# Kernel tuning notes

Measured on AMD Instinct MI355X. Metric: run time of the kernel, lower is better.

The kernel has to match this reference:

```python
import jax, jax.numpy as jnp
import numpy as np

S, B, E = 4096, 8, 1024
H, D, K = 16, 64, 64  # num_heads, head_dim, proj_dim
TAU = 1.0

def setup_inputs() -> dict:
    key = jax.random.key(0)
    ks = jax.random.split(key, 6)
    return {
        "encoder_output": jax.random.normal(ks[0], (S, B, E), dtype=jnp.float32),
        "Wk": jax.random.normal(ks[1], (E, E), dtype=jnp.float32) * (E ** -0.5),
        "bk": jax.random.normal(ks[2], (E,), dtype=jnp.float32) * 0.02,
        "Wv": jax.random.normal(ks[3], (E, E), dtype=jnp.float32) * (E ** -0.5),
        "bv": jax.random.normal(ks[4], (E,), dtype=jnp.float32) * 0.02,
        "random_matrices": jax.random.normal(ks[5], (H, K, D), dtype=jnp.float32),
        "mask": jnp.zeros((S, B, 1, 1), dtype=bool),
    }

def reference(encoder_output, Wk, bk, Wv, bv, random_matrices, mask):
    # k/v projections: [S,B,E] -> [S,B,H,D]
    k = (encoder_output @ Wk.T + bk).reshape(S, B, H, D)
    v = (encoder_output @ Wv.T + bv).reshape(S, B, H, D)
    # build_random_matrices (reparam_proj=False): divide by tau
    rm = random_matrices / TAU
    # rrf random feature map: scale by head_dim**-0.5 / tau, project, sin/cos concat
    x = k * (D ** -0.5) / TAU
    proj = jnp.einsum('sbhd,hkd->sbhk', x, rm)  # [S,B,H,K]
    phi_k = jnp.concatenate([jnp.sin(proj), jnp.cos(proj)], axis=-1) * (K ** -0.5)  # [S,B,H,2K]
    phi_k = jnp.where(mask, 0.0, phi_k)
    # s/z linear-attention state accumulation over seq_len
    s = jnp.einsum('sbhk,sbhd->bhkd', phi_k, v)  # [B,H,2K,D]
    z = jnp.sum(phi_k, axis=0)                   # [B,H,2K]
    return (s, z, rm)
```

## Files before the change

kernel.cpp:

```cpp
#include <hip/hip_runtime.h>
#include <hip/hip_bf16.h>
#include <stdint.h>


typedef short bf16x8 __attribute__((ext_vector_type(8)));
typedef float f32x4 __attribute__((ext_vector_type(4)));

__device__ __forceinline__ unsigned short f2bf(float f) {
  unsigned u = __float_as_uint(f);
  u += 0x7fffu + ((u >> 16) & 1u);
  return (unsigned short)(u >> 16);
}
__device__ __forceinline__ unsigned pack2(float a, float b) {
  return (unsigned)f2bf(a) | ((unsigned)f2bf(b) << 16);
}

#define OFF_WC   0ull
#define OFF_BC   4194304ull
#define OFF_AB   4202496ull
#define OFF_PS   71311360ull
#define OFF_PZ   104865792ull

#define NB_CONV 16384
#define NB_W2   (NB_CONV + 256)
#define NB_WV   (NB_W2 + 512)
#define NB_RM   (NB_WV + 64)
#define NB_ALL  (NB_RM + 1)

__global__ __launch_bounds__(256) void k_pre(const float* __restrict__ enc,
                                             const float* __restrict__ Wk,
                                             const float* __restrict__ bk,
                                             const float* __restrict__ Wv,
                                             const float* __restrict__ bv,
                                             const float* __restrict__ rm,
                                             unsigned short* __restrict__ ab,
                                             unsigned short* __restrict__ Wc,
                                             float* __restrict__ bc,
                                             float* __restrict__ out) {
  const int bid = blockIdx.x;
  const int tid = threadIdx.x;
  if (bid < NB_CONV) {
    const int r = bid * 2 + (tid >> 7);
    const int e = (tid & 127) * 8;
    const int s = r >> 3, b = r & 7;
    const float4* p = (const float4*)(enc + (size_t)r * 1024 + e);
    float4 a = p[0], b4 = p[1];
    uint4 o;
    o.x = pack2(a.x, a.y);  o.y = pack2(a.z, a.w);
    o.z = pack2(b4.x, b4.y); o.w = pack2(b4.z, b4.w);
    *(uint4*)(ab + ((size_t)b * 4096 + s) * 1024 + e) = o;
  } else if (bid < NB_W2) {
    const int t = bid - NB_CONV;
    const int h = t >> 4, et = t & 15;
    __shared__ float Rt[64][65];
    __shared__ float Wt[64][65];
    #pragma unroll
    for (int i = 0; i < 4; ++i) {
      const int fi = i * 256 + tid;
      const int row = fi >> 4, c4 = (fi & 15) * 4;
      float4 w = *(const float4*)(Wk + (size_t)(h * 64 + row) * 1024 + et * 64 + c4);
      Wt[row][c4] = w.x; Wt[row][c4 + 1] = w.y; Wt[row][c4 + 2] = w.z; Wt[row][c4 + 3] = w.w;
      float4 r = *(const float4*)(rm + (size_t)(h * 64 + row) * 64 + c4);
      Rt[row][c4] = r.x * 0.125f; Rt[row][c4 + 1] = r.y * 0.125f;
      Rt[row][c4 + 2] = r.z * 0.125f; Rt[row][c4 + 3] = r.w * 0.125f;
    }
    __syncthreads();
    const int kk = tid & 63, eq = tid >> 6, e0 = eq * 16;
    float accw[16] = {};
    for (int d = 0; d < 64; ++d) {
      const float rv = Rt[kk][d];
      #pragma unroll
      for (int i = 0; i < 16; ++i) accw[i] += rv * Wt[d][e0 + i];
    }
    unsigned short* wout = Wc + (size_t)(h * 64 + kk) * 1024 + et * 64 + e0;
    #pragma unroll
    for (int i2 = 0; i2 < 4; ++i2) {
      uint2 o; o.x = pack2(accw[i2 * 4], accw[i2 * 4 + 1]);
      o.y = pack2(accw[i2 * 4 + 2], accw[i2 * 4 + 3]);
      *(uint2*)(wout + i2 * 4) = o;
    }
    if (et == 0 && tid < 64) {
      float sbb = 0.f;
      for (int d = 0; d < 64; ++d) sbb += Rt[tid][d] * bk[h * 64 + d];
      bc[h * 64 + tid] = sbb;
    }
  } else if (bid < NB_WV) {
    size_t i = ((size_t)(bid - NB_W2) * 256 + tid) * 8;
    const float4* p = (const float4*)(Wv + i);
    float4 a = p[0], b4 = p[1];
    uint4 o;
    o.x = pack2(a.x, a.y);  o.y = pack2(a.z, a.w);
    o.z = pack2(b4.x, b4.y); o.w = pack2(b4.z, b4.w);
    *(uint4*)(Wc + 1048576ull + i) = o;
  } else if (bid < NB_RM) {
    size_t i = ((size_t)(bid - NB_WV) * 256 + tid) * 4;
    *(float4*)(out + 1064960 + i) = *(const float4*)(rm + i);
  } else {
    const int j = tid * 4;
    if (j < 1024) *(float4*)(bc + 1024 + j) = *(const float4*)(bv + j);
  }
}

__device__ __forceinline__ void glds16(const unsigned short* g, unsigned short* l) {
  __builtin_amdgcn_global_load_lds((const __attribute__((address_space(1))) unsigned int*)g,
                                   (__attribute__((address_space(3))) unsigned int*)l,
                                   16, 0, 0);
}

__global__ __launch_bounds__(256, 2) void k_fused(const unsigned short* __restrict__ Ab,
                                                  const unsigned short* __restrict__ Wc,
                                                  const float* __restrict__ bc,
                                                  float* __restrict__ ps,
                                                  float* __restrict__ pz) {
  __shared__ char smem[50176];
  unsigned short* As = (unsigned short*)smem;
  unsigned short* Bs = As + 128 * 64;
  unsigned short* Ph = (unsigned short*)smem;
  unsigned short* Vl = (unsigned short*)(smem + 32768);
  float* zbuf = (float*)(smem + 49152);
  float* Psf  = (float*)smem;

  const int bx = blockIdx.x;
  const int xcd = bx & 7;
  const int idx = bx >> 3;
  const int hp = idx & 7;
  const int g = idx >> 3;
  const int bcg = g * 8 + xcd;
  const int b = bcg >> 3;
  const int sp = bcg & 7;

  const int tid = threadIdx.x;
  const int wave = tid >> 6;
  const int lane = tid & 63;
  const int wm = wave >> 1, wn = wave & 1;
  const int quad = lane >> 4, lm = lane & 15;
  const int lr = lane >> 3;
  const int lc = (((lane & 7) ^ lr) * 8);

  int nrow[4];
  #pragma unroll
  for (int j = 0; j < 4; ++j)
    nrow[j] = (j < 2) ? (wn * 32 + j * 16 + lm) : (64 + wn * 32 + (j - 2) * 16 + lm);
  float biasjh[2][4];
  #pragma unroll
  for (int hi = 0; hi < 2; ++hi) {
    const int h = hp * 2 + hi;
    #pragma unroll
    for (int j = 0; j < 4; ++j)
      biasjh[hi][j] = (j < 2) ? bc[h * 64 + nrow[j]] : bc[1024 + h * 64 + (nrow[j] - 64)];
  }

  f32x4 acc2[2][2][4] = {};
  float zsv[2][2] = {}, zcv[2][2] = {};

  for (int st = 0; st < 4; ++st) {
    const int s_base = sp * 512 + st * 128;
    for (int hi = 0; hi < 2; ++hi) {
      const int h = hp * 2 + hi;
      f32x4 acc[4][4] = {};

      for (int kt = 0; kt < 16; ++kt) {
        const int k0 = kt * 64;
        __syncthreads();
        #pragma unroll
        for (int c = 0; c < 4; ++c) {
          const int r = wave * 32 + c * 8;
          glds16(Ab + ((size_t)b * 4096 + s_base + r + lr) * 1024 + k0 + lc, &As[r * 64]);
          const int rr = r + lr;
          const int wrow = h * 64 + rr + ((rr >= 64) ? 960 : 0);
          glds16(Wc + (size_t)wrow * 1024 + k0 + lc, &Bs[r * 64]);
        }
        __syncthreads();
        #pragma unroll
        for (int ks = 0; ks < 2; ++ks) {
          bf16x8 af[4], bfr[4];
          const int sw = ((ks * 4 + quad) ^ (lm & 7)) * 8;
          #pragma unroll
          for (int i = 0; i < 4; ++i)
            af[i] = *(const bf16x8*)&As[(wm * 64 + i * 16 + lm) * 64 + sw];
          #pragma unroll
          for (int j = 0; j < 4; ++j)
            bfr[j] = *(const bf16x8*)&Bs[nrow[j] * 64 + sw];
          #pragma unroll
          for (int i = 0; i < 4; ++i)
            #pragma unroll
            for (int j = 0; j < 4; ++j)
              acc[i][j] = __builtin_amdgcn_mfma_f32_16x16x32_bf16(af[i], bfr[j], acc[i][j], 0, 0, 0);
        }
      }

      __syncthreads();
      #pragma unroll
      for (int j = 0; j < 4; ++j) {
        #pragma unroll
        for (int i = 0; i < 4; ++i) {
          const int ch = wm * 8 + i * 2 + (quad >> 1);
          const int half = (quad & 1) * 4;
          if (j < 2) {
            const int kk = wn * 32 + j * 16 + lm;
            float sv[4], cv[4];
            #pragma unroll
            for (int r = 0; r < 4; ++r) {
              float p = acc[i][j][r] + biasjh[hi][j];
              __sincosf(p, &sv[r], &cv[r]);
              sv[r] *= 0.125f; cv[r] *= 0.125f;
            }
            zsv[hi][j] += sv[0] + sv[1] + sv[2] + sv[3];
            zcv[hi][j] += cv[0] + cv[1] + cv[2] + cv[3];
            uint2 os; os.x = pack2(sv[0], sv[1]); os.y = pack2(sv[2], sv[3]);
            uint2 oc; oc.x = pack2(cv[0], cv[1]); oc.y = pack2(cv[2], cv[3]);
            const int chs = (ch ^ (kk & 7)) * 8;
            *(uint2*)&Ph[kk * 128 + chs + half] = os;
            *(uint2*)&Ph[(kk + 64) * 128 + chs + half] = oc;
          } else {
            const int d = wn * 32 + (j - 2) * 16 + lm;
            uint2 ov;
            ov.x = pack2(acc[i][j][0] + biasjh[hi][j], acc[i][j][1] + biasjh[hi][j]);
            ov.y = pack2(acc[i][j][2] + biasjh[hi][j], acc[i][j][3] + biasjh[hi][j]);
            *(uint2*)&Vl[d * 128 + ((ch ^ (d & 7)) * 8) + half] = ov;
          }
        }
      }
      __syncthreads();

      #pragma unroll
      for (int ks2 = 0; ks2 < 4; ++ks2) {
        bf16x8 pa[2], vb[4];
        #pragma unroll
        for (int i2 = 0; i2 < 2; ++i2) {
          const int c = wave * 32 + i2 * 16 + lm;
          pa[i2] = *(const bf16x8*)&Ph[c * 128 + (((ks2 * 4 + quad) ^ (c & 7)) * 8)];
        }
        #pragma unroll
        for (int j2 = 0; j2 < 4; ++j2) {
          const int d = j2 * 16 + lm;
          vb[j2] = *(const bf16x8*)&Vl[d * 128 + (((ks2 * 4 + quad) ^ (d & 7)) * 8)];
        }
        #pragma unroll
        for (int i2 = 0; i2 < 2; ++i2)
          #pragma unroll
          for (int j2 = 0; j2 < 4; ++j2)
            acc2[hi][i2][j2] = __builtin_amdgcn_mfma_f32_16x16x32_bf16(pa[i2], vb[j2], acc2[hi][i2][j2], 0, 0, 0);
      }
    }
  }

  #pragma unroll
  for (int hi = 0; hi < 2; ++hi) {
    __syncthreads();
    #pragma unroll
    for (int i2 = 0; i2 < 2; ++i2)
      #pragma unroll
      for (int j2 = 0; j2 < 4; ++j2) {
        const int d = j2 * 16 + lm;
        #pragma unroll
        for (int r = 0; r < 4; ++r) {
          const int c = wave * 32 + i2 * 16 + quad * 4 + r;
          Psf[c * 64 + d] = acc2[hi][i2][j2][r];
        }
      }
    float zsl[2], zcl[2];
    #pragma unroll
    for (int j = 0; j < 2; ++j) {
      zsl[j] = zsv[hi][j]; zcl[j] = zcv[hi][j];
      zsl[j] += __shfl_xor(zsl[j], 16); zsl[j] += __shfl_xor(zsl[j], 32);
      zcl[j] += __shfl_xor(zcl[j], 16); zcl[j] += __shfl_xor(zcl[j], 32);
    }
    if (quad == 0) {
      #pragma unroll
      for (int j = 0; j < 2; ++j) {
        zbuf[wm * 128 + wn * 32 + j * 16 + lm] = zsl[j];
        zbuf[wm * 128 + 64 + wn * 32 + j * 16 + lm] = zcl[j];
      }
    }
    __syncthreads();

    const size_t bh = (size_t)b * 16 + hp * 2 + hi;
    float* po = ps + ((size_t)sp * 128 + bh) * 8192;
    #pragma unroll
    for (int rr = 0; rr < 8; ++rr) {
      const int f = rr * 256 + tid;
      ((float4*)po)[f] = ((const float4*)Psf)[f];
    }
    if (tid < 128)
      pz[((size_t)sp * 128 + bh) * 128 + tid] = zbuf[tid] + zbuf[128 + tid];
  }
}

__global__ __launch_bounds__(256) void k_reduce(const float* __restrict__ ps,
                                                const float* __restrict__ pz,
                                                float* __restrict__ out) {
  size_t i = ((size_t)blockIdx.x * 256 + threadIdx.x) * 4;
  if (i < 1048576) {
    float4 a = {0.f, 0.f, 0.f, 0.f};
    #pragma unroll
    for (int sp = 0; sp < 8; ++sp) {
      float4 x = *(const float4*)(ps + (size_t)sp * 1048576 + i);
      a.x += x.x; a.y += x.y; a.z += x.z; a.w += x.w;
    }
    *(float4*)(out + i) = a;
  } else if (i < 1064960) {
    size_t j = i - 1048576;
    float4 a = {0.f, 0.f, 0.f, 0.f};
    #pragma unroll
    for (int sp = 0; sp < 8; ++sp) {
      float4 x = *(const float4*)(pz + (size_t)sp * 16384 + j);
      a.x += x.x; a.y += x.y; a.z += x.z; a.w += x.w;
    }
    *(float4*)(out + 1048576 + j) = a;
  }
}

extern "C" void kernel_launch(void* const* d_in, const int* in_sizes, int n_in,
                              void* d_out, int out_size, void* d_ws, size_t ws_size,
                              hipStream_t stream) {
  (void)in_sizes; (void)n_in; (void)out_size; (void)ws_size;
  const float* enc = (const float*)d_in[0];
  const float* Wk  = (const float*)d_in[1];
  const float* bk  = (const float*)d_in[2];
  const float* Wv  = (const float*)d_in[3];
  const float* bv  = (const float*)d_in[4];
  const float* rm  = (const float*)d_in[5];
  float* out = (float*)d_out;
  char* ws = (char*)d_ws;
  unsigned short* Wc  = (unsigned short*)(ws + OFF_WC);
  float*          bc  = (float*)(ws + OFF_BC);
  unsigned short* Ab  = (unsigned short*)(ws + OFF_AB);
  float*          psp = (float*)(ws + OFF_PS);
  float*          pzp = (float*)(ws + OFF_PZ);

  hipLaunchKernelGGL(k_pre,    dim3(NB_ALL), dim3(256), 0, stream,
                     enc, Wk, bk, Wv, bv, rm, Ab, Wc, bc, out);
  hipLaunchKernelGGL(k_fused,  dim3(512),    dim3(256), 0, stream, Ab, Wc, bc, psp, pzp);
  hipLaunchKernelGGL(k_reduce, dim3(1040),   dim3(256), 0, stream, psp, pzp, out);
}
```

Measured before the change: 399.5 us.

## Split work per head with 16-way sequence split and atomic reduction into output

Each block now handles one head and 256 sequence rows instead of a head pair and 512 rows, giving 2048 blocks instead of 512. Partial s and z results are added straight into the zeroed output with float atomics. This removes the partial-sum workspace and the separate reduce kernel, and occupancy is raised to 3 blocks per CU with smaller shared memory. In exchange it adds a memset, many scattered atomic adds, and a summation order that is no longer deterministic.

```diff
diff --git a/kernel.cpp b/kernel.cpp
--- a/kernel.cpp
+++ b/kernel.cpp
@@ -18,8 +18,6 @@
 #define OFF_WC   0ull
 #define OFF_BC   4194304ull
 #define OFF_AB   4202496ull
-#define OFF_PS   71311360ull
-#define OFF_PZ   104865792ull
 
 #define NB_CONV 16384
 #define NB_W2   (NB_CONV + 256)
@@ -107,27 +105,24 @@
                                    16, 0, 0);
 }
 
-__global__ __launch_bounds__(256, 2) void k_fused(const unsigned short* __restrict__ Ab,
+__global__ __launch_bounds__(256, 3) void k_fused(const unsigned short* __restrict__ Ab,
                                                   const unsigned short* __restrict__ Wc,
                                                   const float* __restrict__ bc,
-                                                  float* __restrict__ ps,
-                                                  float* __restrict__ pz) {
-  __shared__ char smem[50176];
+                                                  float* __restrict__ out) {
+  __shared__ char smem[49152];
   unsigned short* As = (unsigned short*)smem;
   unsigned short* Bs = As + 128 * 64;
   unsigned short* Ph = (unsigned short*)smem;
   unsigned short* Vl = (unsigned short*)(smem + 32768);
-  float* zbuf = (float*)(smem + 49152);
-  float* Psf  = (float*)smem;
 
   const int bx = blockIdx.x;
   const int xcd = bx & 7;
   const int idx = bx >> 3;
-  const int hp = idx & 7;
-  const int g = idx >> 3;
-  const int bcg = g * 8 + xcd;
-  const int b = bcg >> 3;
-  const int sp = bcg & 7;
+  const int h = idx & 15;
+  const int bcg = (idx >> 4) * 8 + xcd;
+  const int b = bcg >> 4;
+  const int sp = bcg & 15;
+  const size_t bh = (size_t)b * 16 + h;
 
   const int tid = threadIdx.x;
   const int wave = tid >> 6;
@@ -137,177 +132,137 @@
   const int lr = lane >> 3;
   const int lc = (((lane & 7) ^ lr) * 8);
 
+  float biasj[4];
   int nrow[4];
   #pragma unroll
-  for (int j = 0; j < 4; ++j)
-    nrow[j] = (j < 2) ? (wn * 32 + j * 16 + lm) : (64 + wn * 32 + (j - 2) * 16 + lm);
-  float biasjh[2][4];
-  #pragma unroll
-  for (int hi = 0; hi < 2; ++hi) {
-    const int h = hp * 2 + hi;
-    #pragma unroll
-    for (int j = 0; j < 4; ++j)
-      biasjh[hi][j] = (j < 2) ? bc[h * 64 + nrow[j]] : bc[1024 + h * 64 + (nrow[j] - 64)];
-  }
-
-  f32x4 acc2[2][2][4] = {};
-  float zsv[2][2] = {}, zcv[2][2] = {};
-
-  for (int st = 0; st < 4; ++st) {
-    const int s_base = sp * 512 + st * 128;
-    for (int hi = 0; hi < 2; ++hi) {
-      const int h = hp * 2 + hi;
-      f32x4 acc[4][4] = {};
-
-      for (int kt = 0; kt < 16; ++kt) {
-        const int k0 = kt * 64;
-        __syncthreads();
-        #pragma unroll
-        for (int c = 0; c < 4; ++c) {
-          const int r = wave * 32 + c * 8;
-          glds16(Ab + ((size_t)b * 4096 + s_base + r + lr) * 1024 + k0 + lc, &As[r * 64]);
-          const int rr = r + lr;
-          const int wrow = h * 64 + rr + ((rr >= 64) ? 960 : 0);
-          glds16(Wc + (size_t)wrow * 1024 + k0 + lc, &Bs[r * 64]);
-        }
-        __syncthreads();
-        #pragma unroll
-        for (int ks = 0; ks < 2; ++ks) {
-          bf16x8 af[4], bfr[4];
-          const int sw = ((ks * 4 + quad) ^ (lm & 7)) * 8;
-          #pragma unroll
-          for (int i = 0; i < 4; ++i)
-            af[i] = *(const bf16x8*)&As[(wm * 64 + i * 16 + lm) * 64 + sw];
+  for (int j = 0; j < 4; ++j) {
+    if (j < 2) {
+      nrow[j] = wn * 32 + j * 16 + lm;
+      biasj[j] = bc[h * 64 + nrow[j]];
+    } else {
+      nrow[j] = 64 + wn * 32 + (j - 2) * 16 + lm;
+      biasj[j] = bc[1024 + h * 64 + (nrow[j] - 64)];
+    }
+  }
+
+  f32x4 acc2[2][4] = {};
+  float zs[2] = {0.f, 0.f}, zc[2] = {0.f, 0.f};
+
+  for (int st = 0; st < 2; ++st) {
+    const int s_base = sp * 256 + st * 128;
+    f32x4 acc[4][4] = {};
+
+    for (int kt = 0; kt < 16; ++kt) {
+      const int k0 = kt * 64;
+      __syncthreads();
+      #pragma unroll
+      for (int c = 0; c < 4; ++c) {
+        const int r = wave * 32 + c * 8;
+        glds16(Ab + ((size_t)b * 4096 + s_base + r + lr) * 1024 + k0 + lc, &As[r * 64]);
+        const int rr = r + lr;
+        const int wrow = h * 64 + rr + ((rr >= 64) ? 960 : 0);
+        glds16(Wc + (size_t)wrow * 1024 + k0 + lc, &Bs[r * 64]);
+      }
+      __syncthreads();
+      #pragma unroll
+      for (int ks = 0; ks < 2; ++ks) {
+        bf16x8 af[4], bfr[4];
+        const int sw = ((ks * 4 + quad) ^ (lm & 7)) * 8;
+        #pragma unroll
+        for (int i = 0; i < 4; ++i)
+          af[i] = *(const bf16x8*)&As[(wm * 64 + i * 16 + lm) * 64 + sw];
+        #pragma unroll
+        for (int j = 0; j < 4; ++j)
+          bfr[j] = *(const bf16x8*)&Bs[nrow[j] * 64 + sw];
+        #pragma unroll
+        for (int i = 0; i < 4; ++i)
           #pragma unroll
           for (int j = 0; j < 4; ++j)
-            bfr[j] = *(const bf16x8*)&Bs[nrow[j] * 64 + sw];
+            acc[i][j] = __builtin_amdgcn_mfma_f32_16x16x32_bf16(af[i], bfr[j], acc[i][j], 0, 0, 0);
+      }
+    }
+
+    __syncthreads();
+    #pragma unroll
+    for (int j = 0; j < 4; ++j) {
+      #pragma unroll
+      for (int i = 0; i < 4; ++i) {
+        const int ch = wm * 8 + i * 2 + (quad >> 1);
+        const int half = (quad & 1) * 4;
+        if (j < 2) {
+          const int kk = wn * 32 + j * 16 + lm;
+          float sv[4], cv[4];
           #pragma unroll
-          for (int i = 0; i < 4; ++i)
-            #pragma unroll
-            for (int j = 0; j < 4; ++j)
-              acc[i][j] = __builtin_amdgcn_mfma_f32_16x16x32_bf16(af[i], bfr[j], acc[i][j], 0, 0, 0);
+          for (int r = 0; r < 4; ++r) {
+            float p = acc[i][j][r] + biasj[j];
+            __sincosf(p, &sv[r], &cv[r]);
+            sv[r] *= 0.125f; cv[r] *= 0.125f;
+          }
+          zs[j] += sv[0] + sv[1] + sv[2] + sv[3];
+          zc[j] += cv[0] + cv[1] + cv[2] + cv[3];
+          uint2 os; os.x = pack2(sv[0], sv[1]); os.y = pack2(sv[2], sv[3]);
+          uint2 oc; oc.x = pack2(cv[0], cv[1]); oc.y = pack2(cv[2], cv[3]);
+          const int chs = (ch ^ (kk & 7)) * 8;
+          *(uint2*)&Ph[kk * 128 + chs + half] = os;
+          *(uint2*)&Ph[(kk + 64) * 128 + chs + half] = oc;
+        } else {
+          const int d = wn * 32 + (j - 2) * 16 + lm;
+          uint2 ov;
+          ov.x = pack2(acc[i][j][0] + biasj[j], acc[i][j][1] + biasj[j]);
+          ov.y = pack2(acc[i][j][2] + biasj[j], acc[i][j][3] + biasj[j]);
+          *(uint2*)&Vl[d * 128 + ((ch ^ (d & 7)) * 8) + half] = ov;
         }
       }
-
-      __syncthreads();
-      #pragma unroll
-      for (int j = 0; j < 4; ++j) {
-        #pragma unroll
-        for (int i = 0; i < 4; ++i) {
-          const int ch = wm * 8 + i * 2 + (quad >> 1);
-          const int half = (quad & 1) * 4;
-          if (j < 2) {
-            const int kk = wn * 32 + j * 16 + lm;
-            float sv[4], cv[4];
-            #pragma unroll
-            for (int r = 0; r < 4; ++r) {
-              float p = acc[i][j][r] + biasjh[hi][j];
-              __sincosf(p, &sv[r], &cv[r]);
-              sv[r] *= 0.125f; cv[r] *= 0.125f;
-            }
-            zsv[hi][j] += sv[0] + sv[1] + sv[2] + sv[3];
-            zcv[hi][j] += cv[0] + cv[1] + cv[2] + cv[3];
-            uint2 os; os.x = pack2(sv[0], sv[1]); os.y = pack2(sv[2], sv[3]);
-            uint2 oc; oc.x = pack2(cv[0], cv[1]); oc.y = pack2(cv[2], cv[3]);
-            const int chs = (ch ^ (kk & 7)) * 8;
-            *(uint2*)&Ph[kk * 128 + chs + half] = os;
-            *(uint2*)&Ph[(kk + 64) * 128 + chs + half] = oc;
-          } else {
-            const int d = wn * 32 + (j - 2) * 16 + lm;
-            uint2 ov;
-            ov.x = pack2(acc[i][j][0] + biasjh[hi][j], acc[i][j][1] + biasjh[hi][j]);
-            ov.y = pack2(acc[i][j][2] + biasjh[hi][j], acc[i][j][3] + biasjh[hi][j]);
-            *(uint2*)&Vl[d * 128 + ((ch ^ (d & 7)) * 8) + half] = ov;
-          }
-        }
-      }
-      __syncthreads();
-
-      #pragma unroll
-      for (int ks2 = 0; ks2 < 4; ++ks2) {
-        bf16x8 pa[2], vb[4];
-        #pragma unroll
-        for (int i2 = 0; i2 < 2; ++i2) {
-          const int c = wave * 32 + i2 * 16 + lm;
-          pa[i2] = *(const bf16x8*)&Ph[c * 128 + (((ks2 * 4 + quad) ^ (c & 7)) * 8)];
-        }
-        #pragma unroll
-        for (int j2 = 0; j2 < 4; ++j2) {
-          const int d = j2 * 16 + lm;
-          vb[j2] = *(const bf16x8*)&Vl[d * 128 + (((ks2 * 4 + quad) ^ (d & 7)) * 8)];
-        }
-        #pragma unroll
-        for (int i2 = 0; i2 < 2; ++i2)
-          #pragma unroll
-          for (int j2 = 0; j2 < 4; ++j2)
-            acc2[hi][i2][j2] = __builtin_amdgcn_mfma_f32_16x16x32_bf16(pa[i2], vb[j2], acc2[hi][i2][j2], 0, 0, 0);
-      }
-    }
-  }
-
-  #pragma unroll
-  for (int hi = 0; hi < 2; ++hi) {
+    }
     __syncthreads();
-    #pragma unroll
-    for (int i2 = 0; i2 < 2; ++i2)
+
+    #pragma unroll
+    for (int ks2 = 0; ks2 < 4; ++ks2) {
+      bf16x8 pa[2], vb[4];
+      #pragma unroll
+      for (int i2 = 0; i2 < 2; ++i2) {
+        const int c = wave * 32 + i2 * 16 + lm;
+        pa[i2] = *(const bf16x8*)&Ph[c * 128 + (((ks2 * 4 + quad) ^ (c & 7)) * 8)];
+      }
       #pragma unroll
       for (int j2 = 0; j2 < 4; ++j2) {
         const int d = j2 * 16 + lm;
-        #pragma unroll
-        for (int r = 0; r < 4; ++r) {
-          const int c = wave * 32 + i2 * 16 + quad * 4 + r;
-          Psf[c * 64 + d] = acc2[hi][i2][j2][r];
-        }
-      }
-    float zsl[2], zcl[2];
+        vb[j2] = *(const bf16x8*)&Vl[d * 128 + (((ks2 * 4 + quad) ^ (d & 7)) * 8)];
+      }
+      #pragma unroll
+      for (int i2 = 0; i2 < 2; ++i2)
+        #pragma unroll
+        for (int j2 = 0; j2 < 4; ++j2)
+          acc2[i2][j2] = __builtin_amdgcn_mfma_f32_16x16x32_bf16(pa[i2], vb[j2], acc2[i2][j2], 0, 0, 0);
+    }
+  }
+
+  float* po = out + bh * 8192;
+  #pragma unroll
+  for (int i2 = 0; i2 < 2; ++i2)
+    #pragma unroll
+    for (int j2 = 0; j2 < 4; ++j2) {
+      const int d = j2 * 16 + lm;
+      #pragma unroll
+      for (int r = 0; r < 4; ++r) {
+        const int c = wave * 32 + i2 * 16 + quad * 4 + r;
+        atomicAdd(po + (size_t)c * 64 + d, acc2[i2][j2][r]);
+      }
+    }
+
+  #pragma unroll
+  for (int j = 0; j < 2; ++j) {
+    zs[j] += __shfl_xor(zs[j], 16); zs[j] += __shfl_xor(zs[j], 32);
+    zc[j] += __shfl_xor(zc[j], 16); zc[j] += __shfl_xor(zc[j], 32);
+  }
+  if (quad == 0) {
+    float* zo = out + 1048576 + bh * 128;
     #pragma unroll
     for (int j = 0; j < 2; ++j) {
-      zsl[j] = zsv[hi][j]; zcl[j] = zcv[hi][j];
-      zsl[j] += __shfl_xor(zsl[j], 16); zsl[j] += __shfl_xor(zsl[j], 32);
-      zcl[j] += __shfl_xor(zcl[j], 16); zcl[j] += __shfl_xor(zcl[j], 32);
-    }
-    if (quad == 0) {
-      #pragma unroll
-      for (int j = 0; j < 2; ++j) {
-        zbuf[wm * 128 + wn * 32 + j * 16 + lm] = zsl[j];
-        zbuf[wm * 128 + 64 + wn * 32 + j * 16 + lm] = zcl[j];
-      }
-    }
-    __syncthreads();
-
-    const size_t bh = (size_t)b * 16 + hp * 2 + hi;
-    float* po = ps + ((size_t)sp * 128 + bh) * 8192;
-    #pragma unroll
-    for (int rr = 0; rr < 8; ++rr) {
-      const int f = rr * 256 + tid;
-      ((float4*)po)[f] = ((const float4*)Psf)[f];
-    }
-    if (tid < 128)
-      pz[((size_t)sp * 128 + bh) * 128 + tid] = zbuf[tid] + zbuf[128 + tid];
-  }
-}
-
-__global__ __launch_bounds__(256) void k_reduce(const float* __restrict__ ps,
-                                                const float* __restrict__ pz,
-                                                float* __restrict__ out) {
-  size_t i = ((size_t)blockIdx.x * 256 + threadIdx.x) * 4;
-  if (i < 1048576) {
-    float4 a = {0.f, 0.f, 0.f, 0.f};
-    #pragma unroll
-    for (int sp = 0; sp < 8; ++sp) {
-      float4 x = *(const float4*)(ps + (size_t)sp * 1048576 + i);
-      a.x += x.x; a.y += x.y; a.z += x.z; a.w += x.w;
-    }
-    *(float4*)(out + i) = a;
-  } else if (i < 1064960) {
-    size_t j = i - 1048576;
-    float4 a = {0.f, 0.f, 0.f, 0.f};
-    #pragma unroll
-    for (int sp = 0; sp < 8; ++sp) {
-      float4 x = *(const float4*)(pz + (size_t)sp * 16384 + j);
-      a.x += x.x; a.y += x.y; a.z += x.z; a.w += x.w;
-    }
-    *(float4*)(out + 1048576 + j) = a;
+      const int kk = wn * 32 + j * 16 + lm;
+      atomicAdd(zo + kk, zs[j]);
+      atomicAdd(zo + kk + 64, zc[j]);
+    }
   }
 }
 
@@ -326,11 +281,9 @@
   unsigned short* Wc  = (unsigned short*)(ws + OFF_WC);
   float*          bc  = (float*)(ws + OFF_BC);
   unsigned short* Ab  = (unsigned short*)(ws + OFF_AB);
-  float*          psp = (float*)(ws + OFF_PS);
-  float*          pzp = (float*)(ws + OFF_PZ);
-
-  hipLaunchKernelGGL(k_pre,    dim3(NB_ALL), dim3(256), 0, stream,
+
+  hipMemsetAsync(d_out, 0, 1064960ull * 4, stream);
+  hipLaunchKernelGGL(k_pre,   dim3(NB_ALL), dim3(256), 0, stream,
                      enc, Wk, bk, Wv, bv, rm, Ab, Wc, bc, out);
-  hipLaunchKernelGGL(k_fused,  dim3(512),    dim3(256), 0, stream, Ab, Wc, bc, psp, pzp);
-  hipLaunchKernelGGL(k_reduce, dim3(1040),   dim3(256), 0, stream, psp, pzp, out);
-}
+  hipLaunchKernelGGL(k_fused, dim3(2048),   dim3(256), 0, stream, Ab, Wc, bc, out);
+}
```

After: 397.4 us. Within noise of the previous version (-0.5%).
